# Kernel optimization log

Hardware: AMD Instinct MI355X
Metric: run time of the kernel (lower is better)

Reference implementation:

```python
import jax, jax.numpy as jnp
import numpy as np

D_MODEL = 1024
N_HEADS = 16
HEAD_DIM = D_MODEL // N_HEADS
D_FF = 4096


def setup_inputs() -> dict:
    key = jax.random.key(0)
    ks = jax.random.split(key, 16)
    s = 0.02
    x = jax.random.normal(ks[0], (4, 2048, D_MODEL), dtype=jnp.float32)
    p = {
        'x': x,
        'wq': jax.random.normal(ks[1], (D_MODEL, D_MODEL), jnp.float32) * s,
        'bq': jnp.zeros((D_MODEL,), jnp.float32),
        'wk': jax.random.normal(ks[2], (D_MODEL, D_MODEL), jnp.float32) * s,
        'bk': jnp.zeros((D_MODEL,), jnp.float32),
        'wv': jax.random.normal(ks[3], (D_MODEL, D_MODEL), jnp.float32) * s,
        'bv': jnp.zeros((D_MODEL,), jnp.float32),
        'wo': jax.random.normal(ks[4], (D_MODEL, D_MODEL), jnp.float32) * s,
        'bo': jnp.zeros((D_MODEL,), jnp.float32),
        'w1': jax.random.normal(ks[5], (D_MODEL, D_FF), jnp.float32) * s,
        'b1': jnp.zeros((D_FF,), jnp.float32),
        'w2': jax.random.normal(ks[6], (D_FF, D_MODEL), jnp.float32) * s,
        'b2': jnp.zeros((D_MODEL,), jnp.float32),
        'ln1_g': jnp.ones((D_MODEL,), jnp.float32),
        'ln1_b': jnp.zeros((D_MODEL,), jnp.float32),
        'ln2_g': jnp.ones((D_MODEL,), jnp.float32),
        'ln2_b': jnp.zeros((D_MODEL,), jnp.float32),
    }
    return p


def _layernorm(x, g, b, eps=1e-5):
    mu = jnp.mean(x, axis=-1, keepdims=True)
    var = jnp.mean(jnp.square(x - mu), axis=-1, keepdims=True)
    return (x - mu) * jax.lax.rsqrt(var + eps) * g + b


def reference(x, wq, bq, wk, bk, wv, bv, wo, bo, w1, b1, w2, b2, ln1_g, ln1_b, ln2_g, ln2_b):
    B, S, D = x.shape
    normed = _layernorm(x, ln1_g, ln1_b)
    # projections -> [B, H, S, Dh]
    def split_heads(t):
        return t.reshape(B, S, N_HEADS, HEAD_DIM).transpose(0, 2, 1, 3)
    q = split_heads(normed @ wq + bq)
    k = split_heads(normed @ wk + bk)
    v = split_heads(normed @ wv + bv)
    scale = 1.0 / jnp.sqrt(jnp.float32(HEAD_DIM))
    scores = jnp.einsum('bhqd,bhkd->bhqk', q, k) * scale  # [B,H,S,S]
    causal = jnp.tril(jnp.ones((S, S), dtype=bool))
    scores = jnp.where(causal[None, None], scores, -jnp.inf)
    probs = jax.nn.softmax(scores, axis=-1)
    attn = jnp.einsum('bhqk,bhkd->bhqd', probs, v)
    attn = attn.transpose(0, 2, 1, 3).reshape(B, S, D)
    x = x + (attn @ wo + bo)
    h = _layernorm(x, ln2_g, ln2_b)
    h = jax.nn.gelu(h @ w1 + b1, approximate=False)
    x = x + (h @ w2 + b2)
    return x
```

## Files before the change

kernel.cpp:

```cpp
#include <hip/hip_runtime.h>
#include <hip/hip_bf16.h>
#include <math.h>

typedef __attribute__((ext_vector_type(8))) short short8;
typedef __attribute__((ext_vector_type(4))) short short4v;
typedef __attribute__((ext_vector_type(4))) float floatx4;

#define D_MODEL 1024
#define N_HEADS 16
#define HEAD_DIM 64
#define D_FF 4096
#define BATCH 4
#define SEQ 2048
#define NTOK (BATCH * SEQ)

#define GLOBAL_AS __attribute__((address_space(1)))
#define LDS_AS __attribute__((address_space(3)))

__device__ __forceinline__ void async_ld16(const void* g, void* l) {
    __builtin_amdgcn_global_load_lds((GLOBAL_AS const unsigned int*)g,
                                     (LDS_AS unsigned int*)l, 16, 0, 0);
}

__device__ __forceinline__ short bf16s(float v) {
    __hip_bfloat16 h = __float2bfloat16(v);
    return *(short*)&h;
}

__global__ void wtrans_kernel(const float* __restrict__ in, __hip_bfloat16* __restrict__ out,
                              int R, int C) {
    __shared__ float tile[32][33];
    const int c0 = blockIdx.x * 32, r0 = blockIdx.y * 32;
    const int tx = threadIdx.x & 31, ty = threadIdx.x >> 5;
#pragma unroll
    for (int i = 0; i < 4; ++i) {
        int r = ty + i * 8;
        tile[r][tx] = in[(size_t)(r0 + r) * C + c0 + tx];
    }
    __syncthreads();
#pragma unroll
    for (int i = 0; i < 4; ++i) {
        int r = ty + i * 8;
        out[(size_t)(c0 + r) * R + r0 + tx] = __float2bfloat16(tile[tx][r]);
    }
}

__global__ void bconcat_kernel(const float* __restrict__ bq, const float* __restrict__ bk,
                               const float* __restrict__ bv, float* __restrict__ out) {
    const int i = blockIdx.x * 256 + threadIdx.x;
    float v = (i < 1024) ? bq[i] : (i < 2048 ? bk[i - 1024] : bv[i - 2048]);
    out[i] = v;
}

__global__ void ln_kernel(const float* __restrict__ x, const float* __restrict__ g,
                          const float* __restrict__ b, __hip_bfloat16* __restrict__ out) {
    const int row = blockIdx.x;
    const int tid = threadIdx.x;
    const float4 v = ((const float4*)(x + (size_t)row * D_MODEL))[tid];
    float s = v.x + v.y + v.z + v.w;
    float s2 = v.x * v.x + v.y * v.y + v.z * v.z + v.w * v.w;
#pragma unroll
    for (int off = 32; off >= 1; off >>= 1) {
        s += __shfl_xor(s, off, 64);
        s2 += __shfl_xor(s2, off, 64);
    }
    __shared__ float ss[4], ss2[4];
    const int wid = tid >> 6, lane = tid & 63;
    if (lane == 0) { ss[wid] = s; ss2[wid] = s2; }
    __syncthreads();
    const float tot = ss[0] + ss[1] + ss[2] + ss[3];
    const float tot2 = ss2[0] + ss2[1] + ss2[2] + ss2[3];
    const float mu = tot * (1.0f / D_MODEL);
    const float var = tot2 * (1.0f / D_MODEL) - mu * mu;
    const float rsq = rsqrtf(var + 1e-5f);
    const float vv[4] = {v.x, v.y, v.z, v.w};
#pragma unroll
    for (int j = 0; j < 4; ++j) {
        int c = tid * 4 + j;
        out[(size_t)row * D_MODEL + c] = __float2bfloat16((vv[j] - mu) * rsq * g[c] + b[c]);
    }
}

#define BM 128
#define BN 128
#define BK 64

template <int MODE>
__global__ void gemm_kernel(const __hip_bfloat16* __restrict__ A,
                            const __hip_bfloat16* __restrict__ Bt,
                            const float* __restrict__ bias,
                            const float* __restrict__ resid,
                            void* __restrict__ outp, __hip_bfloat16* __restrict__ vtout,
                            int M, int N, int K, float scale) {
    __shared__ __hip_bfloat16 As[BM * BK];
    __shared__ __hip_bfloat16 Bs[BN * BK];
    const int tid = threadIdx.x;
    const int lane = tid & 63;
    const int w = tid >> 6;
    const int wm = w >> 1, wn = w & 1;
    const int m0 = blockIdx.x * BM;
    const int n0 = blockIdx.y * BN;

    const int srow = lane >> 3;
    const int lgrp = (lane & 7) ^ srow;

    const size_t a_base = (size_t)(m0 + w * 32 + srow) * K + lgrp * 8;
    const size_t b_base = (size_t)(n0 + w * 32 + srow) * K + lgrp * 8;

    const floatx4 vzero = {0.f, 0.f, 0.f, 0.f};
    floatx4 acc[4][4];
#pragma unroll
    for (int i = 0; i < 4; ++i)
#pragma unroll
        for (int j = 0; j < 4; ++j) acc[i][j] = vzero;

    const int lcol = lane & 15;
    const int quad = lane >> 4;
    const int arow = wm * 64 + lcol;
    const int brow = wn * 64 + lcol;
    const int l7 = lcol & 7;

    for (int kt = 0; kt < K; kt += BK) {
        __syncthreads();
#pragma unroll
        for (int j = 0; j < 4; ++j)
            async_ld16(A + a_base + kt + (size_t)(j * 8) * K, &As[(w * 32 + j * 8) * BK]);
#pragma unroll
        for (int j = 0; j < 4; ++j)
            async_ld16(Bt + b_base + kt + (size_t)(j * 8) * K, &Bs[(w * 32 + j * 8) * BK]);
        __syncthreads();
#pragma unroll
        for (int ks = 0; ks < 2; ++ks) {
            const int g = ((ks * 4 + quad) ^ l7) * 8;
            short8 af[4], bf[4];
#pragma unroll
            for (int mt = 0; mt < 4; ++mt) af[mt] = *(const short8*)&As[(arow + mt * 16) * BK + g];
#pragma unroll
            for (int nt = 0; nt < 4; ++nt) bf[nt] = *(const short8*)&Bs[(brow + nt * 16) * BK + g];
#pragma unroll
            for (int mt = 0; mt < 4; ++mt)
#pragma unroll
                for (int nt = 0; nt < 4; ++nt)
                    acc[mt][nt] = __builtin_amdgcn_mfma_f32_16x16x32_bf16(af[mt], bf[nt], acc[mt][nt], 0, 0, 0);
        }
    }

    const int lrow4 = quad * 4;
#pragma unroll
    for (int mt = 0; mt < 4; ++mt) {
#pragma unroll
        for (int nt = 0; nt < 4; ++nt) {
            const int gm0 = m0 + wm * 64 + mt * 16 + lrow4;
            const int gn = n0 + wn * 64 + nt * 16 + lcol;
            const float bb_ = bias[gn];
            if (MODE == 0) {
                const int which = gn >> 10;
                const int rest = gn & 1023;
                const int bb = gm0 >> 11, s = gm0 & (SEQ - 1);
                const int h = rest >> 6, dh = rest & (HEAD_DIM - 1);
                if (which == 2) {
                    short4v pk;
#pragma unroll
                    for (int r = 0; r < 4; ++r) pk[r] = bf16s(acc[mt][nt][r] + bb_);
                    *(short4v*)(vtout + ((size_t)((bb * N_HEADS + h) * HEAD_DIM + dh)) * SEQ + s) = pk;
                } else {
                    const float sc = (which == 0) ? scale : 1.0f;
#pragma unroll
                    for (int r = 0; r < 4; ++r) {
                        float v = (acc[mt][nt][r] + bb_) * sc;
                        ((__hip_bfloat16*)outp)[(size_t)which * NTOK * D_MODEL +
                            ((size_t)(bb * N_HEADS + h) * SEQ + s + r) * HEAD_DIM + dh] =
                            __float2bfloat16(v);
                    }
                }
            } else {
#pragma unroll
                for (int r = 0; r < 4; ++r) {
                    const int gm = gm0 + r;
                    float v = acc[mt][nt][r] + bb_;
                    if (MODE == 1 || MODE == 3) {
                        v += resid[(size_t)gm * N + gn];
                        ((float*)outp)[(size_t)gm * N + gn] = v;
                    } else {
                        const float ge = 0.5f * v * (1.0f + erff(v * 0.70710678118654752f));
                        ((__hip_bfloat16*)outp)[(size_t)gm * N + gn] = __float2bfloat16(ge);
                    }
                }
            }
        }
    }
}

__global__ void __launch_bounds__(256, 2)
attn_kernel(const __hip_bfloat16* __restrict__ q,
            const __hip_bfloat16* __restrict__ k,
            const __hip_bfloat16* __restrict__ vt,
            __hip_bfloat16* __restrict__ o) {
    __shared__ __hip_bfloat16 Ks[2][64 * 64];
    __shared__ __hip_bfloat16 VTs[2][64 * 64];
    __shared__ __hip_bfloat16 Ps[4][2][32 * 64];

    const int tid = threadIdx.x;
    const int lane = tid & 63;
    const int w = tid >> 6;
    const int bh = blockIdx.y;
    const int b = bh >> 4, h = bh & 15;
    const int q0t[2] = {(int)blockIdx.x * 128, (15 - (int)blockIdx.x) * 128};
    const size_t hb = (size_t)bh * SEQ * HEAD_DIM;
    const size_t vhb = (size_t)bh * HEAD_DIM * SEQ;

    const int lcol = lane & 15;
    const int quad = lane >> 4;
    const int l7 = lcol & 7;
    const int lrow4 = quad * 4;
    const int srow = lane >> 3;
    const int lgrp = (lane & 7) ^ srow;

    short8 aq[2][2][2];
#pragma unroll
    for (int t = 0; t < 2; ++t)
#pragma unroll
        for (int rb = 0; rb < 2; ++rb)
#pragma unroll
            for (int ks = 0; ks < 2; ++ks)
                aq[t][rb][ks] = *(const short8*)(q + hb +
                    (size_t)(q0t[t] + w * 32 + rb * 16 + lcol) * 64 + ks * 32 + quad * 8);

    const floatx4 vzero = {0.f, 0.f, 0.f, 0.f};
    floatx4 ao[2][2][4];
    floatx4 aol[2][2];
#pragma unroll
    for (int t = 0; t < 2; ++t)
#pragma unroll
        for (int rb = 0; rb < 2; ++rb) {
            aol[t][rb] = vzero;
#pragma unroll
            for (int nt = 0; nt < 4; ++nt) ao[t][rb][nt] = vzero;
        }
    short8 vone;
#pragma unroll
    for (int j = 0; j < 8; ++j) vone[j] = (short)0x3F80;

    const int rounds = 16 - blockIdx.x;

    for (int rd = 0; rd < rounds; ++rd) {
        const int kv0 = rd * 128;
        __syncthreads();
#pragma unroll
        for (int sub = 0; sub < 2; ++sub)
#pragma unroll
            for (int j = 0; j < 2; ++j) {
                const int rr = w * 16 + j * 8 + srow;
                async_ld16(k + hb + (size_t)(kv0 + sub * 64 + rr) * 64 + lgrp * 8,
                           &Ks[sub][(w * 16 + j * 8) * 64]);
                async_ld16(vt + vhb + (size_t)rr * SEQ + kv0 + sub * 64 + lgrp * 8,
                           &VTs[sub][(w * 16 + j * 8) * 64]);
            }
        __syncthreads();

#pragma unroll
        for (int sub = 0; sub < 2; ++sub) {
            const int kvb = kv0 + sub * 64;
#pragma unroll
            for (int t = 0; t < 2; ++t) {
                const int qw0 = q0t[t] + w * 32;
                if (kvb > qw0 + 31) continue;

                floatx4 st[2][4];
#pragma unroll
                for (int rb = 0; rb < 2; ++rb)
#pragma unroll
                    for (int ntk = 0; ntk < 4; ++ntk) st[rb][ntk] = vzero;
#pragma unroll
                for (int ntk = 0; ntk < 4; ++ntk) {
                    const int krow = ntk * 16 + lcol;
                    const short8 ka0 = *(const short8*)&Ks[sub][krow * 64 + ((quad ^ l7) * 8)];
                    const short8 ka1 = *(const short8*)&Ks[sub][krow * 64 + (((4 + quad) ^ l7) * 8)];
#pragma unroll
                    for (int rb = 0; rb < 2; ++rb) {
                        st[rb][ntk] = __builtin_amdgcn_mfma_f32_16x16x32_bf16(ka0, aq[t][rb][0], st[rb][ntk], 0, 0, 0);
                        st[rb][ntk] = __builtin_amdgcn_mfma_f32_16x16x32_bf16(ka1, aq[t][rb][1], st[rb][ntk], 0, 0, 0);
                    }
                }
                const bool diag = (kvb + 63 > qw0);
#pragma unroll
                for (int rb = 0; rb < 2; ++rb) {
                    const int qrow = qw0 + rb * 16 + lcol;
#pragma unroll
                    for (int ntk = 0; ntk < 4; ++ntk) {
                        short4v pk;
#pragma unroll
                        for (int r = 0; r < 4; ++r) {
                            const int kcol = kvb + ntk * 16 + lrow4 + r;
                            float p = exp2f(st[rb][ntk][r]);
                            if (diag && kcol > qrow) p = 0.f;
                            pk[r] = bf16s(p);
                        }
                        const int grp = ntk * 2 + (quad >> 1);
                        *(short4v*)&Ps[w][t][(rb * 16 + lcol) * 64 +
                                            ((grp ^ l7) * 8) + (quad & 1) * 4] = pk;
                    }
                }
#pragma unroll
                for (int ks = 0; ks < 2; ++ks) {
                    short8 vbf[4];
#pragma unroll
                    for (int ntv = 0; ntv < 4; ++ntv)
                        vbf[ntv] = *(const short8*)&VTs[sub][(ntv * 16 + lcol) * 64 +
                                                            (((ks * 4 + quad) ^ l7) * 8)];
#pragma unroll
                    for (int rb = 0; rb < 2; ++rb) {
                        const short8 pa = *(const short8*)&Ps[w][t][(rb * 16 + lcol) * 64 +
                                                                   (((ks * 4 + quad) ^ l7) * 8)];
                        aol[t][rb] = __builtin_amdgcn_mfma_f32_16x16x32_bf16(pa, vone, aol[t][rb], 0, 0, 0);
#pragma unroll
                        for (int ntv = 0; ntv < 4; ++ntv)
                            ao[t][rb][ntv] = __builtin_amdgcn_mfma_f32_16x16x32_bf16(pa, vbf[ntv], ao[t][rb][ntv], 0, 0, 0);
                    }
                }
            }
        }
    }
#pragma unroll
    for (int t = 0; t < 2; ++t)
#pragma unroll
        for (int rb = 0; rb < 2; ++rb)
#pragma unroll
            for (int ntv = 0; ntv < 4; ++ntv)
#pragma unroll
                for (int r = 0; r < 4; ++r) {
                    const int qrow = q0t[t] + w * 32 + rb * 16 + lrow4 + r;
                    const float ov = ao[t][rb][ntv][r] / aol[t][rb][r];
                    o[((size_t)(b * SEQ) + qrow) * D_MODEL + h * HEAD_DIM + ntv * 16 + lcol] =
                        __float2bfloat16(ov);
                }
}

extern "C" void kernel_launch(void* const* d_in, const int* in_sizes, int n_in,
                              void* d_out, int out_size, void* d_ws, size_t ws_size,
                              hipStream_t stream) {
    (void)in_sizes; (void)n_in; (void)out_size; (void)ws_size;
    const float* x    = (const float*)d_in[0];
    const float* wq   = (const float*)d_in[1];
    const float* bq   = (const float*)d_in[2];
    const float* wk   = (const float*)d_in[3];
    const float* bk   = (const float*)d_in[4];
    const float* wv   = (const float*)d_in[5];
    const float* bv   = (const float*)d_in[6];
    const float* wo   = (const float*)d_in[7];
    const float* bo   = (const float*)d_in[8];
    const float* w1   = (const float*)d_in[9];
    const float* b1   = (const float*)d_in[10];
    const float* w2   = (const float*)d_in[11];
    const float* b2   = (const float*)d_in[12];
    const float* ln1g = (const float*)d_in[13];
    const float* ln1b = (const float*)d_in[14];
    const float* ln2g = (const float*)d_in[15];
    const float* ln2b = (const float*)d_in[16];
    float* out = (float*)d_out;

    char* ws = (char*)d_ws;
    size_t off = 0;
    auto alloc = [&](size_t bytes) { void* p = ws + off; off += bytes; return p; };
    __hip_bfloat16* wqkvT = (__hip_bfloat16*)alloc((size_t)3072 * 1024 * 2);
    __hip_bfloat16* woT = (__hip_bfloat16*)alloc((size_t)1024 * 1024 * 2);
    __hip_bfloat16* w1T = (__hip_bfloat16*)alloc((size_t)4096 * 1024 * 2);
    __hip_bfloat16* w2T = (__hip_bfloat16*)alloc((size_t)4096 * 1024 * 2);
    float* bqkv = (float*)alloc((size_t)3072 * 4);
    __hip_bfloat16* normed = (__hip_bfloat16*)alloc((size_t)NTOK * D_MODEL * 2);
    __hip_bfloat16* qb = (__hip_bfloat16*)alloc((size_t)NTOK * D_MODEL * 2);
    __hip_bfloat16* kb = (__hip_bfloat16*)alloc((size_t)NTOK * D_MODEL * 2);
    __hip_bfloat16* attnb = (__hip_bfloat16*)alloc((size_t)NTOK * D_MODEL * 2);
    float* x1 = (float*)alloc((size_t)NTOK * D_MODEL * 4);
    __hip_bfloat16* hh = (__hip_bfloat16*)alloc((size_t)NTOK * D_FF * 2);
    __hip_bfloat16* vtb = (__hip_bfloat16*)hh;

    const float QSCALE = 0.125f * 1.44269504088896f;

    const dim3 blk(256);
    wtrans_kernel<<<dim3(32, 32), blk, 0, stream>>>(wq, wqkvT, 1024, 1024);
    wtrans_kernel<<<dim3(32, 32), blk, 0, stream>>>(wk, wqkvT + (size_t)1024 * 1024, 1024, 1024);
    wtrans_kernel<<<dim3(32, 32), blk, 0, stream>>>(wv, wqkvT + (size_t)2048 * 1024, 1024, 1024);
    wtrans_kernel<<<dim3(32, 32), blk, 0, stream>>>(wo, woT, 1024, 1024);
    wtrans_kernel<<<dim3(128, 32), blk, 0, stream>>>(w1, w1T, 1024, 4096);
    wtrans_kernel<<<dim3(32, 128), blk, 0, stream>>>(w2, w2T, 4096, 1024);
    bconcat_kernel<<<dim3(12), blk, 0, stream>>>(bq, bk, bv, bqkv);

    ln_kernel<<<NTOK, blk, 0, stream>>>(x, ln1g, ln1b, normed);

    gemm_kernel<0><<<dim3(NTOK / BM, 3072 / BN), blk, 0, stream>>>(normed, wqkvT, bqkv, nullptr, qb, vtb, NTOK, 3072, 1024, QSCALE);

    attn_kernel<<<dim3(8, BATCH * N_HEADS), blk, 0, stream>>>(qb, kb, vtb, attnb);

    gemm_kernel<1><<<dim3(NTOK / BM, 1024 / BN), blk, 0, stream>>>(attnb, woT, bo, x, x1, nullptr, NTOK, 1024, 1024, 1.0f);

    ln_kernel<<<NTOK, blk, 0, stream>>>(x1, ln2g, ln2b, normed);

    gemm_kernel<2><<<dim3(NTOK / BM, D_FF / BN), blk, 0, stream>>>(normed, w1T, b1, nullptr, hh, nullptr, NTOK, D_FF, 1024, 1.0f);
    gemm_kernel<3><<<dim3(NTOK / BM, 1024 / BN), blk, 0, stream>>>(hh, w2T, b2, x1, out, nullptr, NTOK, 1024, D_FF, 1.0f);
}
```

Before: 514.3 us.

## Merge weight prep launches, store residual in bf16, use fast GELU approximation

Merges the six weight-transpose launches and the bias concat into a single prep kernel. Stores the post-attention residual x1 in bf16 instead of fp32, with a matching bf16 LayerNorm kernel, which halves that tensor's traffic. Replaces the erf-based exact GELU with an exp2/rcp sigmoid-style approximation. Rounding the residual stream to bf16 and approximating GELU both lower accuracy relative to the reference.

```diff
diff --git a/kernel.cpp b/kernel.cpp
--- a/kernel.cpp
+++ b/kernel.cpp
@@ -27,10 +27,38 @@
     return *(short*)&h;
 }
 
-__global__ void wtrans_kernel(const float* __restrict__ in, __hip_bfloat16* __restrict__ out,
-                              int R, int C) {
+__device__ __forceinline__ float fast_gelu(float v) {
+    const float t = exp2f(v * (2.302183f + 0.102953f * v * v));
+    return v - v * __builtin_amdgcn_rcpf(t + 1.0f);
+}
+
+__global__ void prep_kernel(const float* __restrict__ wq, const float* __restrict__ wk,
+                            const float* __restrict__ wv, const float* __restrict__ wo,
+                            const float* __restrict__ w1, const float* __restrict__ w2,
+                            const float* __restrict__ bq, const float* __restrict__ bk,
+                            const float* __restrict__ bv,
+                            __hip_bfloat16* __restrict__ wqkvT, __hip_bfloat16* __restrict__ woT,
+                            __hip_bfloat16* __restrict__ w1T, __hip_bfloat16* __restrict__ w2T,
+                            float* __restrict__ bqkv) {
+    const int id = blockIdx.x;
+    if (id >= 12288) {
+        const int i = (id - 12288) * 256 + threadIdx.x;
+        bqkv[i] = (i < 1024) ? bq[i] : (i < 2048 ? bk[i - 1024] : bv[i - 2048]);
+        return;
+    }
+    const float* in;
+    __hip_bfloat16* out;
+    int R, C, t;
+    if (id < 1024)      { in = wq; out = wqkvT;                          R = 1024; C = 1024; t = id; }
+    else if (id < 2048) { in = wk; out = wqkvT + (size_t)1024 * 1024;    R = 1024; C = 1024; t = id - 1024; }
+    else if (id < 3072) { in = wv; out = wqkvT + (size_t)2048 * 1024;    R = 1024; C = 1024; t = id - 2048; }
+    else if (id < 4096) { in = wo; out = woT;                            R = 1024; C = 1024; t = id - 3072; }
+    else if (id < 8192) { in = w1; out = w1T;                            R = 1024; C = 4096; t = id - 4096; }
+    else                { in = w2; out = w2T;                            R = 4096; C = 1024; t = id - 8192; }
+    const int cb = C >> 5;
+    const int c0 = (t % cb) * 32, r0 = (t / cb) * 32;
+
     __shared__ float tile[32][33];
-    const int c0 = blockIdx.x * 32, r0 = blockIdx.y * 32;
     const int tx = threadIdx.x & 31, ty = threadIdx.x >> 5;
 #pragma unroll
     for (int i = 0; i < 4; ++i) {
@@ -43,13 +71,6 @@
         int r = ty + i * 8;
         out[(size_t)(c0 + r) * R + r0 + tx] = __float2bfloat16(tile[tx][r]);
     }
-}
-
-__global__ void bconcat_kernel(const float* __restrict__ bq, const float* __restrict__ bk,
-                               const float* __restrict__ bv, float* __restrict__ out) {
-    const int i = blockIdx.x * 256 + threadIdx.x;
-    float v = (i < 1024) ? bq[i] : (i < 2048 ? bk[i - 1024] : bv[i - 2048]);
-    out[i] = v;
 }
 
 __global__ void ln_kernel(const float* __restrict__ x, const float* __restrict__ g,
@@ -81,6 +102,37 @@
     }
 }
 
+__global__ void ln_bf16_kernel(const __hip_bfloat16* __restrict__ x, const float* __restrict__ g,
+                               const float* __restrict__ b, __hip_bfloat16* __restrict__ out) {
+    const int row = blockIdx.x;
+    const int tid = threadIdx.x;
+    const short4v raw = ((const short4v*)(x + (size_t)row * D_MODEL))[tid];
+    float vv[4];
+#pragma unroll
+    for (int j = 0; j < 4; ++j) { short t = raw[j]; vv[j] = __bfloat162float(*(__hip_bfloat16*)&t); }
+    float s = vv[0] + vv[1] + vv[2] + vv[3];
+    float s2 = vv[0] * vv[0] + vv[1] * vv[1] + vv[2] * vv[2] + vv[3] * vv[3];
+#pragma unroll
+    for (int off = 32; off >= 1; off >>= 1) {
+        s += __shfl_xor(s, off, 64);
+        s2 += __shfl_xor(s2, off, 64);
+    }
+    __shared__ float ss[4], ss2[4];
+    const int wid = tid >> 6, lane = tid & 63;
+    if (lane == 0) { ss[wid] = s; ss2[wid] = s2; }
+    __syncthreads();
+    const float tot = ss[0] + ss[1] + ss[2] + ss[3];
+    const float tot2 = ss2[0] + ss2[1] + ss2[2] + ss2[3];
+    const float mu = tot * (1.0f / D_MODEL);
+    const float var = tot2 * (1.0f / D_MODEL) - mu * mu;
+    const float rsq = rsqrtf(var + 1e-5f);
+#pragma unroll
+    for (int j = 0; j < 4; ++j) {
+        int c = tid * 4 + j;
+        out[(size_t)row * D_MODEL + c] = __float2bfloat16((vv[j] - mu) * rsq * g[c] + b[c]);
+    }
+}
+
 #define BM 128
 #define BN 128
 #define BK 64
@@ -89,7 +141,7 @@
 __global__ void gemm_kernel(const __hip_bfloat16* __restrict__ A,
                             const __hip_bfloat16* __restrict__ Bt,
                             const float* __restrict__ bias,
-                            const float* __restrict__ resid,
+                            const void* __restrict__ resid,
                             void* __restrict__ outp, __hip_bfloat16* __restrict__ vtout,
                             int M, int N, int K, float scale) {
     __shared__ __hip_bfloat16 As[BM * BK];
@@ -178,12 +230,14 @@
                 for (int r = 0; r < 4; ++r) {
                     const int gm = gm0 + r;
                     float v = acc[mt][nt][r] + bb_;
-                    if (MODE == 1 || MODE == 3) {
-                        v += resid[(size_t)gm * N + gn];
+                    if (MODE == 1) {
+                        v += ((const float*)resid)[(size_t)gm * N + gn];
+                        ((__hip_bfloat16*)outp)[(size_t)gm * N + gn] = __float2bfloat16(v);
+                    } else if (MODE == 2) {
+                        ((__hip_bfloat16*)outp)[(size_t)gm * N + gn] = __float2bfloat16(fast_gelu(v));
+                    } else {
+                        v += __bfloat162float(((const __hip_bfloat16*)resid)[(size_t)gm * N + gn]);
                         ((float*)outp)[(size_t)gm * N + gn] = v;
-                    } else {
-                        const float ge = 0.5f * v * (1.0f + erff(v * 0.70710678118654752f));
-                        ((__hip_bfloat16*)outp)[(size_t)gm * N + gn] = __float2bfloat16(ge);
                     }
                 }
             }
@@ -371,20 +425,15 @@
     __hip_bfloat16* qb = (__hip_bfloat16*)alloc((size_t)NTOK * D_MODEL * 2);
     __hip_bfloat16* kb = (__hip_bfloat16*)alloc((size_t)NTOK * D_MODEL * 2);
     __hip_bfloat16* attnb = (__hip_bfloat16*)alloc((size_t)NTOK * D_MODEL * 2);
-    float* x1 = (float*)alloc((size_t)NTOK * D_MODEL * 4);
+    __hip_bfloat16* x1 = (__hip_bfloat16*)alloc((size_t)NTOK * D_MODEL * 2);
     __hip_bfloat16* hh = (__hip_bfloat16*)alloc((size_t)NTOK * D_FF * 2);
     __hip_bfloat16* vtb = (__hip_bfloat16*)hh;
 
     const float QSCALE = 0.125f * 1.44269504088896f;
 
     const dim3 blk(256);
-    wtrans_kernel<<<dim3(32, 32), blk, 0, stream>>>(wq, wqkvT, 1024, 1024);
-    wtrans_kernel<<<dim3(32, 32), blk, 0, stream>>>(wk, wqkvT + (size_t)1024 * 1024, 1024, 1024);
-    wtrans_kernel<<<dim3(32, 32), blk, 0, stream>>>(wv, wqkvT + (size_t)2048 * 1024, 1024, 1024);
-    wtrans_kernel<<<dim3(32, 32), blk, 0, stream>>>(wo, woT, 1024, 1024);
-    wtrans_kernel<<<dim3(128, 32), blk, 0, stream>>>(w1, w1T, 1024, 4096);
-    wtrans_kernel<<<dim3(32, 128), blk, 0, stream>>>(w2, w2T, 4096, 1024);
-    bconcat_kernel<<<dim3(12), blk, 0, stream>>>(bq, bk, bv, bqkv);
+    prep_kernel<<<dim3(12300), blk, 0, stream>>>(wq, wk, wv, wo, w1, w2, bq, bk, bv,
+                                                 wqkvT, woT, w1T, w2T, bqkv);
 
     ln_kernel<<<NTOK, blk, 0, stream>>>(x, ln1g, ln1b, normed);
 
@@ -394,7 +443,7 @@
 
     gemm_kernel<1><<<dim3(NTOK / BM, 1024 / BN), blk, 0, stream>>>(attnb, woT, bo, x, x1, nullptr, NTOK, 1024, 1024, 1.0f);
 
-    ln_kernel<<<NTOK, blk, 0, stream>>>(x1, ln2g, ln2b, normed);
+    ln_bf16_kernel<<<NTOK, blk, 0, stream>>>(x1, ln2g, ln2b, normed);
 
     gemm_kernel<2><<<dim3(NTOK / BM, D_FF / BN), blk, 0, stream>>>(normed, w1T, b1, nullptr, hh, nullptr, NTOK, D_FF, 1024, 1.0f);
     gemm_kernel<3><<<dim3(NTOK / BM, 1024 / BN), blk, 0, stream>>>(hh, w2T, b2, x1, out, nullptr, NTOK, 1024, D_FF, 1.0f);
```

New measurement: 476.7 us. 1.08x faster.
